# Optimization experiments

Measured on AMD Instinct MI355X. Metric: run time of the kernel, lower is better.

Reference implementation:

```python
import jax, jax.numpy as jnp
import numpy as np

H = 16          # num_attention_heads
HD = 64         # hidden_size_per_attention_head
EPS = 1e-12

def _layernorm(x, w, b):
    u = x.mean(-1, keepdims=True)
    s = ((x - u) ** 2).mean(-1, keepdims=True)
    return w * (x - u) / jnp.sqrt(s + EPS) + b

def _split_heads(x):
    b, s, d = x.shape
    return x.reshape(b, s, H, d // H).transpose(0, 2, 1, 3)  # [b,h,s,hd]

def _merge_heads(x):
    b, h, s, hd = x.shape
    return x.transpose(0, 2, 1, 3).reshape(b, s, h * hd)


def setup_inputs() -> dict:
    key = jax.random.key(0)
    ks = jax.random.split(key, 20)
    B, S, T, D, F = 4, 1024, 1024, 1024, 4096
    w = lambda k, shp: (jax.random.normal(k, shp, jnp.float32) * 0.02)
    return {
        "hidden_states": jax.random.normal(ks[0], (B, S, D), jnp.float32),
        "enc_hidden_states": jax.random.normal(ks[1], (B, T, D), jnp.float32),
        "enc_attn_mask": jnp.zeros((B, 1, 1, T), jnp.float32),
        "dec_attn_mask": jnp.tril(jnp.ones((S, S), jnp.float32)).reshape(1, 1, S, S),
        "ln1_w": jnp.ones((D,), jnp.float32), "ln1_b": jnp.zeros((D,), jnp.float32),
        "qkv_w": w(ks[2], (D, 3 * D)), "qkv_b": jnp.zeros((3 * D,), jnp.float32),
        "attn_o_w": w(ks[3], (D, D)), "attn_o_b": jnp.zeros((D,), jnp.float32),
        "ln2_w": jnp.ones((D,), jnp.float32), "ln2_b": jnp.zeros((D,), jnp.float32),
        "q_w": w(ks[4], (D, D)), "q_b": jnp.zeros((D,), jnp.float32),
        "kv_w": w(ks[5], (D, 2 * D)), "kv_b": jnp.zeros((2 * D,), jnp.float32),
        "ca_o_w": w(ks[6], (D, D)), "ca_o_b": jnp.zeros((D,), jnp.float32),
        "ln3_w": jnp.ones((D,), jnp.float32), "ln3_b": jnp.zeros((D,), jnp.float32),
        "ffn_in_w": w(ks[7], (D, F)), "ffn_in_b": jnp.zeros((F,), jnp.float32),
        "ffn_out_w": w(ks[8], (F, D)), "ffn_out_b": jnp.zeros((D,), jnp.float32),
    }


def reference(hidden_states, enc_hidden_states, enc_attn_mask, dec_attn_mask,
              ln1_w, ln1_b, qkv_w, qkv_b, attn_o_w, attn_o_b,
              ln2_w, ln2_b, q_w, q_b, kv_w, kv_b, ca_o_w, ca_o_b,
              ln3_w, ln3_b, ffn_in_w, ffn_in_b, ffn_out_w, ffn_out_b):
    scale = 1.0 / jnp.sqrt(jnp.float32(HD))
    # dropout layers are identity (eval mode)

    # ---- self-attention (ltor multiplicative mask formula) ----
    residual = hidden_states
    x = _layernorm(hidden_states, ln1_w, ln1_b)
    qkv = x @ qkv_w + qkv_b
    q, k, v = jnp.split(qkv, 3, axis=-1)
    q, k, v = _split_heads(q), _split_heads(k), _split_heads(v)
    scores = jnp.einsum('bhsd,bhtd->bhst', q, k) * scale
    scores = scores * dec_attn_mask - 10000.0 * (1.0 - dec_attn_mask)
    probs = jax.nn.softmax(scores, axis=-1)
    ctx = _merge_heads(jnp.einsum('bhst,bhtd->bhsd', probs, v))
    hidden_states = residual + (ctx @ attn_o_w + attn_o_b)

    # ---- cross-attention (additive enc mask) ----
    residual = hidden_states
    x = _layernorm(hidden_states, ln2_w, ln2_b)
    q = _split_heads(x @ q_w + q_b)
    kv = enc_hidden_states @ kv_w + kv_b
    k, v = jnp.split(kv, 2, axis=-1)
    k, v = _split_heads(k), _split_heads(v)
    scores = jnp.einsum('bhsd,bhtd->bhst', q, k) * scale + enc_attn_mask
    probs = jax.nn.softmax(scores, axis=-1)
    ctx = _merge_heads(jnp.einsum('bhst,bhtd->bhsd', probs, v))
    hidden_states = residual + (ctx @ ca_o_w + ca_o_b)

    # ---- FFN ----
    residual = hidden_states
    x = _layernorm(hidden_states, ln3_w, ln3_b)
    x = jax.nn.gelu(x @ ffn_in_w + ffn_in_b, approximate=False)
    x = x @ ffn_out_w + ffn_out_b
    return residual + x
```

## Files before the change

kernel.cpp:

```cpp
#include <hip/hip_runtime.h>
#include <cstdint>
#include <cstddef>

typedef unsigned short u16;
typedef __bf16 bf16x8 __attribute__((ext_vector_type(8)));
typedef float f32x4 __attribute__((ext_vector_type(4)));

__device__ __forceinline__ u16 f2bf(float f) {
  unsigned u = __float_as_uint(f);
  u += 0x7fffu + ((u >> 16) & 1u);
  return (u16)(u >> 16);
}

__device__ __forceinline__ float block_sum(float v, float* sbuf, int tid) {
#pragma unroll
  for (int off = 1; off < 64; off <<= 1) v += __shfl_xor(v, off, 64);
  if ((tid & 63) == 0) sbuf[tid >> 6] = v;
  __syncthreads();
  v = sbuf[0] + sbuf[1] + sbuf[2] + sbuf[3];
  __syncthreads();
  return v;
}

__device__ __forceinline__ void gld16(const void* g, void* l) {
  __builtin_amdgcn_global_load_lds((const __attribute__((address_space(1))) void*)g,
                                   (__attribute__((address_space(3))) void*)l,
                                   16, 0, 0);
}

__device__ __forceinline__ void swz(int& bx, int& by) {
  const int gx = gridDim.x, gy = gridDim.y;
  const int id = blockIdx.y * gx + blockIdx.x;
  const int xcd = id & 7, slot = id >> 3;
  bx = xcd * (gx >> 3) + slot / gy;
  by = slot % gy;
}


#define GEMM_SETUP(Kdim)                                                         \
  const int lane = tid & 63, wave = tid >> 6;                                    \
  const int l15 = lane & 15, g = (lane >> 4) & 3;                                \
  const int wm = (wave >> 1) * 64, wn = (wave & 1) * 64;                         \
  const int c0 = tid, c1 = tid + 256;                                            \
  const int ar0 = c0 >> 2, ak0 = (c0 & 3) * 8;                                   \
  const int ar1 = c1 >> 2, ak1 = (c1 & 3) * 8;                                   \
  const size_t aoff0 = (size_t)(m0 + ar0) * Kdim + ak0;                          \
  const size_t aoff1 = (size_t)(m0 + ar1) * Kdim + ak1;                          \
  const size_t boff0 = (size_t)(n0 + ar0) * Kdim + ak0;                          \
  const size_t boff1 = (size_t)(n0 + ar1) * Kdim + ak1;

#define GEMM_STAGE(Aptr, Bptr, kk, buf)                                          \
    gld16(Aptr + aoff0 + (kk), As + (buf) * 4096 + (size_t)c0 * 8);              \
    gld16(Aptr + aoff1 + (kk), As + (buf) * 4096 + (size_t)c1 * 8);              \
    gld16(Bptr + boff0 + (kk), Bs + (buf) * 4096 + (size_t)c0 * 8);              \
    gld16(Bptr + boff1 + (kk), Bs + (buf) * 4096 + (size_t)c1 * 8);

#define GEMM_COMPUTE(buf)                                                        \
    { bf16x8 af[4], bg[4];                                                       \
      _Pragma("unroll")                                                          \
      for (int i = 0; i < 4; i++) {                                              \
        af[i] = *(const bf16x8*)(As + (buf) * 4096 + (wm + i * 16 + l15) * 32 + g * 8); \
        bg[i] = *(const bf16x8*)(Bs + (buf) * 4096 + (wn + i * 16 + l15) * 32 + g * 8); \
      }                                                                          \
      _Pragma("unroll")                                                          \
      for (int i = 0; i < 4; i++)                                                \
        _Pragma("unroll")                                                        \
        for (int j = 0; j < 4; j++)                                              \
          acc[i][j] = __builtin_amdgcn_mfma_f32_16x16x32_bf16(af[i], bg[j], acc[i][j], 0, 0, 0); }

#define GEMM_BODY_DB(Aptr, Bptr, Kdim)                                           \
  GEMM_SETUP(Kdim)                                                               \
  f32x4 acc[4][4] = {};                                                          \
  GEMM_STAGE(Aptr, Bptr, kstart, 0)                                              \
  int cur = 0;                                                                   \
  for (int k0 = kstart; k0 + 32 < kend; k0 += 32) {                              \
    GEMM_STAGE(Aptr, Bptr, k0 + 32, cur ^ 1)                                     \
    asm volatile("s_waitcnt vmcnt(4)\ns_barrier" ::: "memory");                  \
    GEMM_COMPUTE(cur)                                                            \
    asm volatile("s_waitcnt lgkmcnt(0)\ns_barrier" ::: "memory");                \
    cur ^= 1;                                                                    \
  }                                                                              \
  asm volatile("s_waitcnt vmcnt(0)\ns_barrier" ::: "memory");                    \
  GEMM_COMPUTE(cur)

template<int BM, int MODE>
__global__ __launch_bounds__(512, 2) void gemm_big(
    const u16* __restrict__ A, const u16* __restrict__ B,
    const float* __restrict__ bias,
    u16* __restrict__ out0, u16* __restrict__ out1, u16* __restrict__ out2,
    int N, int K)
{
  constexpr int NQA = BM / 64;
  constexpr int IF  = BM / 32;
  __shared__ __align__(16) u16 As[2 * BM * 64];
  __shared__ __align__(16) u16 Bs[2 * 256 * 64];

  const int tid = threadIdx.x;
  const int lane = tid & 63, wave = tid >> 6;
  const int l15 = lane & 15, g = (lane >> 4) & 3;
  const int wr = (wave >> 2) * (BM / 2), wc = (wave & 3) * 64;

  const int gx = gridDim.x;
  const int nwg = gx * gridDim.y;
  const int id = blockIdx.y * gx + blockIdx.x;
  const int qq = nwg >> 3, rr = nwg & 7;
  const int xcd = id & 7, slot = id >> 3;
  const int sid = (xcd < rr ? xcd * (qq + 1) : rr * (qq + 1) + (xcd - rr) * qq) + slot;
  const int bx = sid % gx, by = sid / gx;
  const int m0 = by * BM, n0 = bx * 256;

  size_t aoff[NQA]; int adst[NQA];
  size_t boff[4];   int bdst[4];
#pragma unroll
  for (int q = 0; q < NQA; ++q) {
    const int c = tid + q * 512, row = c >> 3, ch = (c & 7) ^ (row & 7);
    aoff[q] = (size_t)(m0 + row) * K + ch * 8;
    adst[q] = c * 8;
  }
#pragma unroll
  for (int q = 0; q < 4; ++q) {
    const int c = tid + q * 512, row = c >> 3, ch = (c & 7) ^ (row & 7);
    boff[q] = (size_t)(n0 + row) * K + ch * 8;
    bdst[q] = c * 8;
  }

#define G2_STAGE(kk, buf)                                                        \
  {                                                                              \
    _Pragma("unroll")                                                            \
    for (int q = 0; q < NQA; ++q) gld16(A + aoff[q] + (kk), As + (buf) * (BM * 64) + adst[q]); \
    _Pragma("unroll")                                                            \
    for (int q = 0; q < 4; ++q)  gld16(B + boff[q] + (kk), Bs + (buf) * 16384 + bdst[q]); \
  }

#define G2_COMPUTE(buf)                                                          \
  {                                                                              \
    _Pragma("unroll")                                                            \
    for (int ks = 0; ks < 2; ++ks) {                                             \
      const int chR = (((ks * 4 + g) ^ (l15 & 7)) * 8);                          \
      bf16x8 af[IF], bg[4];                                                      \
      _Pragma("unroll")                                                          \
      for (int i = 0; i < IF; ++i)                                               \
        af[i] = *(const bf16x8*)(As + (buf) * (BM * 64) + (wr + i * 16 + l15) * 64 + chR); \
      _Pragma("unroll")                                                          \
      for (int j = 0; j < 4; ++j)                                                \
        bg[j] = *(const bf16x8*)(Bs + (buf) * 16384 + (wc + j * 16 + l15) * 64 + chR); \
      _Pragma("unroll")                                                          \
      for (int i = 0; i < IF; ++i)                                               \
        _Pragma("unroll")                                                        \
        for (int j = 0; j < 4; ++j)                                              \
          acc[i][j] = __builtin_amdgcn_mfma_f32_16x16x32_bf16(af[i], bg[j], acc[i][j], 0, 0, 0); \
    }                                                                            \
  }

  f32x4 acc[IF][4] = {};
  const int NT = K >> 6;
  G2_STAGE(0, 0)
  int cur = 0;
  for (int t = 0; t < NT - 1; ++t) {
    G2_STAGE((t + 1) * 64, cur ^ 1)
    if constexpr (BM == 256) asm volatile("s_waitcnt vmcnt(8)\ns_barrier" ::: "memory");
    else                     asm volatile("s_waitcnt vmcnt(6)\ns_barrier" ::: "memory");
    G2_COMPUTE(cur)
    asm volatile("s_waitcnt lgkmcnt(0)\ns_barrier" ::: "memory");
    cur ^= 1;
  }
  asm volatile("s_waitcnt vmcnt(0)\ns_barrier" ::: "memory");
  G2_COMPUTE(cur)

#undef G2_STAGE
#undef G2_COMPUTE

  if constexpr (MODE == 0) {
#pragma unroll
    for (int i = 0; i < IF; ++i) {
#pragma unroll
      for (int j = 0; j < 4; ++j) {
        const int col = n0 + wc + j * 16 + l15;
        const float bs = bias[col];
#pragma unroll
        for (int r = 0; r < 4; ++r) {
          const int gm = m0 + wr + i * 16 + g * 4 + r;
          float v = acc[i][j][r] + bs;
          v = 0.5f * v * (1.0f + erff(v * 0.70710678118654752f));
          out0[(size_t)gm * N + col] = f2bf(v);
        }
      }
    }
  } else {
#pragma unroll
    for (int i = 0; i < IF; ++i) {
#pragma unroll
      for (int j = 0; j < 4; ++j) {
        const int col = n0 + wc + j * 16 + l15;
        const int sec = (n0 + wc + j * 16) >> 10;
        const int tgt = (MODE == 1) ? sec : sec + 1;
        const float bs = bias[col];
#pragma unroll
        for (int r = 0; r < 4; ++r) {
          const int gm = m0 + wr + i * 16 + g * 4 + r;
          const float v = acc[i][j][r] + bs;
          const int cl = col & 1023, h = cl >> 6, d = cl & 63;
          const int z = (gm >> 10) * 16 + h, s = gm & 1023;
          if (tgt == 0)
            out0[((size_t)z * 1024 + s) * 64 + d] = f2bf(v * 0.125f);
          else if (tgt == 1)
            out1[((((size_t)z * 8 + (s >> 7)) * 8 + (d >> 3)) * 128 + (s & 127)) * 8 + (d & 7)] = f2bf(v);
          else
            out2[((size_t)z * 8 + (s >> 7)) * 8192 + (((s >> 3) & 15) * 64 + d) * 8 + (s & 7)] = f2bf(v);
        }
      }
    }
  }
}

__global__ __launch_bounds__(256) void gemm_splitk(
    const u16* __restrict__ A, const u16* __restrict__ B,
    float* __restrict__ part, int K, int Klen)
{
  __shared__ __align__(16) u16 As[2 * 128 * 32];
  __shared__ __align__(16) u16 Bs[2 * 128 * 32];
  const int tid = threadIdx.x;
  int bx, by; swz(bx, by);
  const int m0 = by * 128, n0 = bx * 128;
  const int kstart = blockIdx.z * Klen, kend = kstart + Klen;
  float* outP = part + (size_t)blockIdx.z * (4096ULL * 1024);
  GEMM_BODY_DB(A, B, K)

#pragma unroll
  for (int i = 0; i < 4; i++)
#pragma unroll
    for (int j = 0; j < 4; j++) {
      const int col = n0 + wn + j * 16 + l15;
#pragma unroll
      for (int r = 0; r < 4; r++) {
        const int gm = m0 + wm + i * 16 + g * 4 + r;
        outP[(size_t)gm * 1024 + col] = acc[i][j][r];
      }
    }
}

__global__ __launch_bounds__(256, 2) void flash_attn(
    const u16* __restrict__ qh, const u16* __restrict__ kt, const u16* __restrict__ vt,
    const float* __restrict__ emask, u16* __restrict__ ctx, int causal)
{
  __shared__ __align__(16) u16 sK[8192];
  __shared__ __align__(16) u16 sV[8192];
  __shared__ __align__(16) u16 sP[128 * 72];

  const int tid = threadIdx.x, lane = tid & 63, wave = tid >> 6;
  const int l15 = lane & 15, g = (lane >> 4) & 3;
  const int id = blockIdx.y * 8 + blockIdx.x;
  const int xcd = id & 7, slot = id >> 3;
  const int z = xcd * 8 + (slot >> 3), b = z >> 4, h = z & 15;
  const int m0 = (slot & 7) * 128;
  const int r0 = wave * 32;

  bf16x8 qf[2][2];
  {
    const u16* qz = qh + ((size_t)z * 1024 + m0 + r0 + l15) * 64 + g * 8;
#pragma unroll
    for (int i2 = 0; i2 < 2; ++i2)
#pragma unroll
      for (int kc = 0; kc < 2; ++kc)
        qf[i2][kc] = *(const bf16x8*)(qz + (size_t)i2 * 16 * 64 + kc * 32);
  }

  float m_i[2][4], l_i[2][4];
#pragma unroll
  for (int i2 = 0; i2 < 2; ++i2)
#pragma unroll
    for (int r = 0; r < 4; ++r) { m_i[i2][r] = -1.0e30f; l_i[i2][r] = 0.0f; }

  f32x4 o[2][4] = {};
  const int tmax = causal ? m0 : 896;

  for (int t0 = 0; t0 <= tmax; t0 += 128) {
    const u16* ktile = kt + ((size_t)z * 8 + (t0 >> 7)) * 8192;
    const u16* vtile = vt + ((size_t)z * 8 + (t0 >> 7)) * 8192;
    __syncthreads();
#pragma unroll
    for (int i = 0; i < 4; ++i) {
      const int off = (wave * 4 + i) * 512 + lane * 8;
      gld16(ktile + off, sK + off);
      gld16(vtile + off, sV + off);
    }
    __syncthreads();

#pragma unroll
    for (int ci = 0; ci < 2; ++ci) {
      if (causal && t0 == m0 && ci * 64 > r0 + 31) continue;

      f32x4 sa[2][4] = {};
#pragma unroll
      for (int kc = 0; kc < 2; ++kc) {
        bf16x8 bg[4];
#pragma unroll
        for (int jn = 0; jn < 4; ++jn)
          bg[jn] = *(const bf16x8*)(sK + ((kc * 4 + g) * 128 + ci * 64 + jn * 16 + l15) * 8);
#pragma unroll
        for (int i2 = 0; i2 < 2; ++i2)
#pragma unroll
          for (int jn = 0; jn < 4; ++jn)
            sa[i2][jn] = __builtin_amdgcn_mfma_f32_16x16x32_bf16(qf[i2][kc], bg[jn], sa[i2][jn], 0, 0, 0);
      }

      if (causal) {
        if (t0 == m0 && ci * 64 + 63 > r0) {
#pragma unroll
          for (int i2 = 0; i2 < 2; ++i2)
#pragma unroll
            for (int jn = 0; jn < 4; ++jn) {
              const int col = ci * 64 + jn * 16 + l15;
#pragma unroll
              for (int r = 0; r < 4; ++r) {
                const int row = r0 + i2 * 16 + g * 4 + r;
                if (col > row) sa[i2][jn][r] = -3.0e38f;
              }
            }
        }
      } else {
#pragma unroll
        for (int jn = 0; jn < 4; ++jn) {
          const float mv = emask[(size_t)b * 1024 + t0 + ci * 64 + jn * 16 + l15];
#pragma unroll
          for (int i2 = 0; i2 < 2; ++i2)
#pragma unroll
            for (int r = 0; r < 4; ++r) sa[i2][jn][r] += mv;
        }
      }

      float alpha[2][4];
#pragma unroll
      for (int i2 = 0; i2 < 2; ++i2)
#pragma unroll
        for (int r = 0; r < 4; ++r) {
          const int rowl = r0 + i2 * 16 + g * 4 + r;
          float v = fmaxf(fmaxf(sa[i2][0][r], sa[i2][1][r]), fmaxf(sa[i2][2][r], sa[i2][3][r]));
          v = fmaxf(v, __shfl_xor(v, 1, 64));
          v = fmaxf(v, __shfl_xor(v, 2, 64));
          v = fmaxf(v, __shfl_xor(v, 4, 64));
          v = fmaxf(v, __shfl_xor(v, 8, 64));
          const float mo = m_i[i2][r];
          const float mn = fmaxf(mo, v);
          m_i[i2][r] = mn;
          alpha[i2][r] = __expf(mo - mn);
          float s = 0.0f;
#pragma unroll
          for (int jn = 0; jn < 4; ++jn) {
            const float p = __expf(sa[i2][jn][r] - mn);
            s += p;
            sP[rowl * 72 + jn * 16 + l15] = f2bf(p);
          }
          s += __shfl_xor(s, 1, 64);
          s += __shfl_xor(s, 2, 64);
          s += __shfl_xor(s, 4, 64);
          s += __shfl_xor(s, 8, 64);
          l_i[i2][r] = alpha[i2][r] * l_i[i2][r] + s;
        }

#pragma unroll
      for (int i2 = 0; i2 < 2; ++i2)
#pragma unroll
        for (int jn = 0; jn < 4; ++jn)
#pragma unroll
          for (int r = 0; r < 4; ++r)
            o[i2][jn][r] *= alpha[i2][r];

      asm volatile("s_waitcnt lgkmcnt(0)" ::: "memory");
#pragma unroll
      for (int kc2 = 0; kc2 < 2; ++kc2) {
        bf16x8 pa[2], vb[4];
#pragma unroll
        for (int i2 = 0; i2 < 2; ++i2)
          pa[i2] = *(const bf16x8*)(sP + (r0 + i2 * 16 + l15) * 72 + kc2 * 32 + g * 8);
#pragma unroll
        for (int jn = 0; jn < 4; ++jn)
          vb[jn] = *(const bf16x8*)(sV + ((ci * 8 + kc2 * 4 + g) * 64 + jn * 16 + l15) * 8);
#pragma unroll
        for (int i2 = 0; i2 < 2; ++i2)
#pragma unroll
          for (int jn = 0; jn < 4; ++jn)
            o[i2][jn] = __builtin_amdgcn_mfma_f32_16x16x32_bf16(pa[i2], vb[jn], o[i2][jn], 0, 0, 0);
      }
    }
  }

#pragma unroll
  for (int i2 = 0; i2 < 2; ++i2)
#pragma unroll
    for (int r = 0; r < 4; ++r) {
      const float inv = 1.0f / l_i[i2][r];
      const size_t base = ((size_t)(b * 1024 + m0 + r0 + i2 * 16 + g * 4 + r)) * 1024 + h * 64;
#pragma unroll
      for (int jn = 0; jn < 4; ++jn)
        ctx[base + jn * 16 + l15] = f2bf(o[i2][jn][r] * inv);
    }
}

struct PrepArgs {
  const float* w[7]; u16* wt[7]; int K[7]; int N[7]; int cum[7];
  const float* enc; u16* enc_bf;
  const float* hid; const float* ln1w; const float* ln1b; u16* xln;
};
__global__ __launch_bounds__(256) void prep_kernel(PrepArgs a) {
  __shared__ float t[32][33];
  __shared__ float sbuf[4];
  const int bb = blockIdx.x, tid = threadIdx.x;
  if (bb < 16384) {
    int wi = 0;
#pragma unroll
    for (int i = 0; i < 7; ++i) if (bb >= a.cum[i]) wi = i + 1; else break;
    const int base = wi ? a.cum[wi - 1] : 0;
    const int tileIdx = bb - base;
    const int Kd = a.K[wi], Nd = a.N[wi], nx = Nd >> 5;
    const int n0 = (tileIdx % nx) * 32, k0 = (tileIdx / nx) * 32;
    const float* w = a.w[wi]; u16* wt = a.wt[wi];
    const int tx = tid & 31, ty = tid >> 5;
#pragma unroll
    for (int r = ty; r < 32; r += 8) t[r][tx] = w[(size_t)(k0 + r) * Nd + n0 + tx];
    __syncthreads();
#pragma unroll
    for (int r = ty; r < 32; r += 8) wt[(size_t)(n0 + r) * Kd + k0 + tx] = f2bf(t[tx][r]);
  } else if (bb < 20480) {
    const size_t i = ((size_t)(bb - 16384) * 256 + tid) * 4;
    const float4 v = *(const float4*)(a.enc + i);
    ushort4 o; o.x = f2bf(v.x); o.y = f2bf(v.y); o.z = f2bf(v.z); o.w = f2bf(v.w);
    *(ushort4*)(a.enc_bf + i) = o;
  } else {
    const int row = bb - 20480;
    const float4 v = *(const float4*)(a.hid + (size_t)row * 1024 + tid * 4);
    float s = block_sum(v.x + v.y + v.z + v.w, sbuf, tid);
    const float u = s * (1.0f / 1024.0f);
    const float d0 = v.x - u, d1 = v.y - u, d2 = v.z - u, d3 = v.w - u;
    float sq = block_sum(d0 * d0 + d1 * d1 + d2 * d2 + d3 * d3, sbuf, tid);
    const float rstd = rsqrtf(sq * (1.0f / 1024.0f) + 1e-12f);
    const int c = tid * 4;
    ushort4 o;
    o.x = f2bf(a.ln1w[c + 0] * d0 * rstd + a.ln1b[c + 0]);
    o.y = f2bf(a.ln1w[c + 1] * d1 * rstd + a.ln1b[c + 1]);
    o.z = f2bf(a.ln1w[c + 2] * d2 * rstd + a.ln1b[c + 2]);
    o.w = f2bf(a.ln1w[c + 3] * d3 * rstd + a.ln1b[c + 3]);
    *(ushort4*)(a.xln + (size_t)row * 1024 + c) = o;
  }
}

__global__ __launch_bounds__(256) void ln_red_kernel(
    const float* __restrict__ p0, const float* __restrict__ p1,
    const float* __restrict__ bias, const float* __restrict__ res,
    const float* __restrict__ w, const float* __restrict__ b,
    float* __restrict__ hOut, u16* __restrict__ xln)
{
  __shared__ float sbuf[4];
  const int row = blockIdx.x, tid = threadIdx.x;
  const size_t off = (size_t)row * 1024 + tid * 4;
  const int c = tid * 4;
  const float4 a0 = *(const float4*)(p0 + off);
  const float4 a1 = *(const float4*)(p1 + off);
  const float4 bs = *(const float4*)(bias + c);
  const float4 rs = *(const float4*)(res + off);
  float4 v;
  v.x = a0.x + a1.x + bs.x + rs.x;
  v.y = a0.y + a1.y + bs.y + rs.y;
  v.z = a0.z + a1.z + bs.z + rs.z;
  v.w = a0.w + a1.w + bs.w + rs.w;
  *(float4*)(hOut + off) = v;
  float s = block_sum(v.x + v.y + v.z + v.w, sbuf, tid);
  const float u = s * (1.0f / 1024.0f);
  const float d0 = v.x - u, d1 = v.y - u, d2 = v.z - u, d3 = v.w - u;
  float sq = block_sum(d0 * d0 + d1 * d1 + d2 * d2 + d3 * d3, sbuf, tid);
  const float rstd = rsqrtf(sq * (1.0f / 1024.0f) + 1e-12f);
  ushort4 o;
  o.x = f2bf(w[c + 0] * d0 * rstd + b[c + 0]);
  o.y = f2bf(w[c + 1] * d1 * rstd + b[c + 1]);
  o.z = f2bf(w[c + 2] * d2 * rstd + b[c + 2]);
  o.w = f2bf(w[c + 3] * d3 * rstd + b[c + 3]);
  *(ushort4*)(xln + off) = o;
}

__global__ __launch_bounds__(256) void reduce_q_kernel(
    const float* __restrict__ p0, const float* __restrict__ p1,
    const float* __restrict__ bias, u16* __restrict__ qh)
{
  const int m = blockIdx.x, tid = threadIdx.x;
  const size_t off = (size_t)m * 1024 + tid * 4;
  const int n = tid * 4, h = n >> 6, d = n & 63;
  const int b = m >> 10, s = m & 1023;
  const float4 a0 = *(const float4*)(p0 + off);
  const float4 a1 = *(const float4*)(p1 + off);
  const float4 bs = *(const float4*)(bias + n);
  ushort4 o;
  o.x = f2bf((a0.x + a1.x + bs.x) * 0.125f);
  o.y = f2bf((a0.y + a1.y + bs.y) * 0.125f);
  o.z = f2bf((a0.z + a1.z + bs.z) * 0.125f);
  o.w = f2bf((a0.w + a1.w + bs.w) * 0.125f);
  *(ushort4*)(qh + ((size_t)((b * 16 + h) * 1024 + s)) * 64 + d) = o;
}

__global__ __launch_bounds__(256) void reduce_out_kernel(
    const float* __restrict__ p0, const float* __restrict__ p1,
    const float* __restrict__ bias, const float* __restrict__ res,
    float* __restrict__ out)
{
  const int m = blockIdx.x, tid = threadIdx.x;
  const size_t off = (size_t)m * 1024 + tid * 4;
  const int c = tid * 4;
  const float4 a0 = *(const float4*)(p0 + off);
  const float4 a1 = *(const float4*)(p1 + off);
  const float4 bs = *(const float4*)(bias + c);
  const float4 rs = *(const float4*)(res + off);
  float4 v;
  v.x = a0.x + a1.x + bs.x + rs.x;
  v.y = a0.y + a1.y + bs.y + rs.y;
  v.z = a0.z + a1.z + bs.z + rs.z;
  v.w = a0.w + a1.w + bs.w + rs.w;
  *(float4*)(out + off) = v;
}

constexpr size_t MB = 1024ULL * 1024;
constexpr size_t WT_QKV    = 0;
constexpr size_t WT_ATTN_O = 6 * MB;
constexpr size_t WT_Q      = 8 * MB;
constexpr size_t WT_KV     = 10 * MB;
constexpr size_t WT_CA_O   = 14 * MB;
constexpr size_t WT_FFN_IN = 16 * MB;
constexpr size_t WT_FFN_OUT= 24 * MB;
constexpr size_t ENC_BF    = 32 * MB;
constexpr size_t XLN       = 40 * MB;
constexpr size_t QH        = 48 * MB;
constexpr size_t KT        = 56 * MB;
constexpr size_t VT        = 64 * MB;
constexpr size_t CTX       = 72 * MB;
constexpr size_t HBUF      = 80 * MB;
constexpr size_t SP0       = 96 * MB;
constexpr size_t SP1       = 112 * MB;
constexpr size_t FFN_MID   = 128 * MB;

extern "C" void kernel_launch(void* const* d_in, const int* in_sizes, int n_in,
                              void* d_out, int out_size, void* d_ws, size_t ws_size,
                              hipStream_t stream) {
  const float* hidden   = (const float*)d_in[0];
  const float* enc      = (const float*)d_in[1];
  const float* encm     = (const float*)d_in[2];
  const float* ln1w = (const float*)d_in[4],  *ln1b = (const float*)d_in[5];
  const float* qkv_w = (const float*)d_in[6], *qkv_b = (const float*)d_in[7];
  const float* attn_o_w = (const float*)d_in[8], *attn_o_b = (const float*)d_in[9];
  const float* ln2w = (const float*)d_in[10], *ln2b = (const float*)d_in[11];
  const float* q_w = (const float*)d_in[12],  *q_b = (const float*)d_in[13];
  const float* kv_w = (const float*)d_in[14], *kv_b = (const float*)d_in[15];
  const float* ca_o_w = (const float*)d_in[16], *ca_o_b = (const float*)d_in[17];
  const float* ln3w = (const float*)d_in[18], *ln3b = (const float*)d_in[19];
  const float* ffn_in_w = (const float*)d_in[20], *ffn_in_b = (const float*)d_in[21];
  const float* ffn_out_w = (const float*)d_in[22], *ffn_out_b = (const float*)d_in[23];

  char* ws = (char*)d_ws;
  u16* wt_qkv    = (u16*)(ws + WT_QKV);
  u16* wt_attn_o = (u16*)(ws + WT_ATTN_O);
  u16* wt_q      = (u16*)(ws + WT_Q);
  u16* wt_kv     = (u16*)(ws + WT_KV);
  u16* wt_ca_o   = (u16*)(ws + WT_CA_O);
  u16* wt_ffn_in = (u16*)(ws + WT_FFN_IN);
  u16* wt_ffn_out= (u16*)(ws + WT_FFN_OUT);
  u16* enc_bf = (u16*)(ws + ENC_BF);
  u16* xln    = (u16*)(ws + XLN);
  u16* qh     = (u16*)(ws + QH);
  u16* kt     = (u16*)(ws + KT);
  u16* vt     = (u16*)(ws + VT);
  u16* ctx    = (u16*)(ws + CTX);
  float* hF   = (float*)(ws + HBUF);
  float* sp0  = (float*)(ws + SP0);
  float* sp1  = (float*)(ws + SP1);
  u16* ffn_mid = (u16*)(ws + FFN_MID);

  PrepArgs pa;
  pa.w[0] = qkv_w;    pa.wt[0] = wt_qkv;     pa.K[0] = 1024; pa.N[0] = 3072; pa.cum[0] = 3072;
  pa.w[1] = attn_o_w; pa.wt[1] = wt_attn_o;  pa.K[1] = 1024; pa.N[1] = 1024; pa.cum[1] = 4096;
  pa.w[2] = q_w;      pa.wt[2] = wt_q;       pa.K[2] = 1024; pa.N[2] = 1024; pa.cum[2] = 5120;
  pa.w[3] = kv_w;     pa.wt[3] = wt_kv;      pa.K[3] = 1024; pa.N[3] = 2048; pa.cum[3] = 7168;
  pa.w[4] = ca_o_w;   pa.wt[4] = wt_ca_o;    pa.K[4] = 1024; pa.N[4] = 1024; pa.cum[4] = 8192;
  pa.w[5] = ffn_in_w; pa.wt[5] = wt_ffn_in;  pa.K[5] = 1024; pa.N[5] = 4096; pa.cum[5] = 12288;
  pa.w[6] = ffn_out_w;pa.wt[6] = wt_ffn_out; pa.K[6] = 4096; pa.N[6] = 1024; pa.cum[6] = 16384;
  pa.enc = enc; pa.enc_bf = enc_bf;
  pa.hid = hidden; pa.ln1w = ln1w; pa.ln1b = ln1b; pa.xln = xln;
  prep_kernel<<<24576, 256, 0, stream>>>(pa);

  gemm_big<256, 1><<<dim3(12, 16), 512, 0, stream>>>(xln, wt_qkv, qkv_b, qh, kt, vt, 3072, 1024);
  flash_attn<<<dim3(8, 64), 256, 0, stream>>>(qh, kt, vt, nullptr, ctx, 1);
  gemm_splitk<<<dim3(8, 32, 2), 256, 0, stream>>>(ctx, wt_attn_o, sp0, 1024, 512);
  ln_red_kernel<<<4096, 256, 0, stream>>>(sp0, sp1, attn_o_b, hidden, ln2w, ln2b, hF, xln);

  gemm_splitk<<<dim3(8, 32, 2), 256, 0, stream>>>(xln, wt_q, sp0, 1024, 512);
  reduce_q_kernel<<<4096, 256, 0, stream>>>(sp0, sp1, q_b, qh);
  gemm_big<128, 3><<<dim3(8, 32), 512, 0, stream>>>(enc_bf, wt_kv, kv_b, nullptr, kt, vt, 2048, 1024);
  flash_attn<<<dim3(8, 64), 256, 0, stream>>>(qh, kt, vt, encm, ctx, 0);
  gemm_splitk<<<dim3(8, 32, 2), 256, 0, stream>>>(ctx, wt_ca_o, sp0, 1024, 512);
  ln_red_kernel<<<4096, 256, 0, stream>>>(sp0, sp1, ca_o_b, hF, ln3w, ln3b, hF, xln);

  gemm_big<256, 0><<<dim3(16, 16), 512, 0, stream>>>(xln, wt_ffn_in, ffn_in_b, ffn_mid, nullptr, nullptr, 4096, 1024);
  gemm_splitk<<<dim3(8, 32, 2), 256, 0, stream>>>(ffn_mid, wt_ffn_out, sp0, 4096, 2048);
  reduce_out_kernel<<<4096, 256, 0, stream>>>(sp0, sp1, ffn_out_b, hF, (float*)d_out);
}
```

Baseline: 581.0 us.

## Replace 128x128 split-K GEMMs with big-tile swizzled GEMM, drop split-K for D×D

The old 128x128, K=32 split-K kernel is replaced by a templated gemm_part that reuses the big-GEMM machinery: 512 threads, a 256-column tile, K=64 steps with XOR-swizzled LDS and XCD-aware block remapping. The three D×D projections now run without split-K (BM=64, 256 blocks), so the reduction kernels read a single partial buffer instead of summing two. The FFN-out GEMM keeps a 2-way split with BM=128. Fewer blocks and no split for the small GEMMs lower parallelism, traded against less partial-buffer traffic and better reuse per tile.

```diff
diff --git a/kernel.cpp b/kernel.cpp
--- a/kernel.cpp
+++ b/kernel.cpp
@@ -28,111 +28,47 @@
                                    16, 0, 0);
 }
 
-__device__ __forceinline__ void swz(int& bx, int& by) {
-  const int gx = gridDim.x, gy = gridDim.y;
-  const int id = blockIdx.y * gx + blockIdx.x;
-  const int xcd = id & 7, slot = id >> 3;
-  bx = xcd * (gx >> 3) + slot / gy;
-  by = slot % gy;
-}
-
-
-#define GEMM_SETUP(Kdim)                                                         \
+
+
+#define BIG_PREAMBLE(BM, Kdim, KB)                                               \
+  constexpr int NQA = (BM) / 64;                                                 \
+  constexpr int IF  = (BM) / 32;                                                 \
+  const int tid = threadIdx.x;                                                   \
   const int lane = tid & 63, wave = tid >> 6;                                    \
   const int l15 = lane & 15, g = (lane >> 4) & 3;                                \
-  const int wm = (wave >> 1) * 64, wn = (wave & 1) * 64;                         \
-  const int c0 = tid, c1 = tid + 256;                                            \
-  const int ar0 = c0 >> 2, ak0 = (c0 & 3) * 8;                                   \
-  const int ar1 = c1 >> 2, ak1 = (c1 & 3) * 8;                                   \
-  const size_t aoff0 = (size_t)(m0 + ar0) * Kdim + ak0;                          \
-  const size_t aoff1 = (size_t)(m0 + ar1) * Kdim + ak1;                          \
-  const size_t boff0 = (size_t)(n0 + ar0) * Kdim + ak0;                          \
-  const size_t boff1 = (size_t)(n0 + ar1) * Kdim + ak1;
-
-#define GEMM_STAGE(Aptr, Bptr, kk, buf)                                          \
-    gld16(Aptr + aoff0 + (kk), As + (buf) * 4096 + (size_t)c0 * 8);              \
-    gld16(Aptr + aoff1 + (kk), As + (buf) * 4096 + (size_t)c1 * 8);              \
-    gld16(Bptr + boff0 + (kk), Bs + (buf) * 4096 + (size_t)c0 * 8);              \
-    gld16(Bptr + boff1 + (kk), Bs + (buf) * 4096 + (size_t)c1 * 8);
-
-#define GEMM_COMPUTE(buf)                                                        \
-    { bf16x8 af[4], bg[4];                                                       \
-      _Pragma("unroll")                                                          \
-      for (int i = 0; i < 4; i++) {                                              \
-        af[i] = *(const bf16x8*)(As + (buf) * 4096 + (wm + i * 16 + l15) * 32 + g * 8); \
-        bg[i] = *(const bf16x8*)(Bs + (buf) * 4096 + (wn + i * 16 + l15) * 32 + g * 8); \
-      }                                                                          \
-      _Pragma("unroll")                                                          \
-      for (int i = 0; i < 4; i++)                                                \
-        _Pragma("unroll")                                                        \
-        for (int j = 0; j < 4; j++)                                              \
-          acc[i][j] = __builtin_amdgcn_mfma_f32_16x16x32_bf16(af[i], bg[j], acc[i][j], 0, 0, 0); }
-
-#define GEMM_BODY_DB(Aptr, Bptr, Kdim)                                           \
-  GEMM_SETUP(Kdim)                                                               \
-  f32x4 acc[4][4] = {};                                                          \
-  GEMM_STAGE(Aptr, Bptr, kstart, 0)                                              \
-  int cur = 0;                                                                   \
-  for (int k0 = kstart; k0 + 32 < kend; k0 += 32) {                              \
-    GEMM_STAGE(Aptr, Bptr, k0 + 32, cur ^ 1)                                     \
-    asm volatile("s_waitcnt vmcnt(4)\ns_barrier" ::: "memory");                  \
-    GEMM_COMPUTE(cur)                                                            \
-    asm volatile("s_waitcnt lgkmcnt(0)\ns_barrier" ::: "memory");                \
-    cur ^= 1;                                                                    \
+  const int wr = (wave >> 2) * ((BM) / 2), wc = (wave & 3) * 64;                 \
+  const int gx = gridDim.x;                                                      \
+  const int nwg = gx * gridDim.y;                                                \
+  const int id = blockIdx.y * gx + blockIdx.x;                                   \
+  const int qq = nwg >> 3, rr = nwg & 7;                                         \
+  const int xcd = id & 7, slot = id >> 3;                                        \
+  const int sid = (xcd < rr ? xcd * (qq + 1) : rr * (qq + 1) + (xcd - rr) * qq) + slot; \
+  const int bx = sid % gx, by = sid / gx;                                        \
+  const int m0 = by * (BM), n0 = bx * 256;                                       \
+  size_t aoff[NQA]; int adst[NQA];                                               \
+  size_t boff[4];   int bdst[4];                                                 \
+  _Pragma("unroll")                                                              \
+  for (int q = 0; q < NQA; ++q) {                                                \
+    const int c = tid + q * 512, row = c >> 3, ch = (c & 7) ^ (row & 7);         \
+    aoff[q] = (size_t)(m0 + row) * (Kdim) + ch * 8 + (KB);                       \
+    adst[q] = c * 8;                                                             \
   }                                                                              \
-  asm volatile("s_waitcnt vmcnt(0)\ns_barrier" ::: "memory");                    \
-  GEMM_COMPUTE(cur)
-
-template<int BM, int MODE>
-__global__ __launch_bounds__(512, 2) void gemm_big(
-    const u16* __restrict__ A, const u16* __restrict__ B,
-    const float* __restrict__ bias,
-    u16* __restrict__ out0, u16* __restrict__ out1, u16* __restrict__ out2,
-    int N, int K)
-{
-  constexpr int NQA = BM / 64;
-  constexpr int IF  = BM / 32;
-  __shared__ __align__(16) u16 As[2 * BM * 64];
-  __shared__ __align__(16) u16 Bs[2 * 256 * 64];
-
-  const int tid = threadIdx.x;
-  const int lane = tid & 63, wave = tid >> 6;
-  const int l15 = lane & 15, g = (lane >> 4) & 3;
-  const int wr = (wave >> 2) * (BM / 2), wc = (wave & 3) * 64;
-
-  const int gx = gridDim.x;
-  const int nwg = gx * gridDim.y;
-  const int id = blockIdx.y * gx + blockIdx.x;
-  const int qq = nwg >> 3, rr = nwg & 7;
-  const int xcd = id & 7, slot = id >> 3;
-  const int sid = (xcd < rr ? xcd * (qq + 1) : rr * (qq + 1) + (xcd - rr) * qq) + slot;
-  const int bx = sid % gx, by = sid / gx;
-  const int m0 = by * BM, n0 = bx * 256;
-
-  size_t aoff[NQA]; int adst[NQA];
-  size_t boff[4];   int bdst[4];
-#pragma unroll
-  for (int q = 0; q < NQA; ++q) {
-    const int c = tid + q * 512, row = c >> 3, ch = (c & 7) ^ (row & 7);
-    aoff[q] = (size_t)(m0 + row) * K + ch * 8;
-    adst[q] = c * 8;
-  }
-#pragma unroll
-  for (int q = 0; q < 4; ++q) {
-    const int c = tid + q * 512, row = c >> 3, ch = (c & 7) ^ (row & 7);
-    boff[q] = (size_t)(n0 + row) * K + ch * 8;
-    bdst[q] = c * 8;
-  }
-
-#define G2_STAGE(kk, buf)                                                        \
+  _Pragma("unroll")                                                              \
+  for (int q = 0; q < 4; ++q) {                                                  \
+    const int c = tid + q * 512, row = c >> 3, ch = (c & 7) ^ (row & 7);         \
+    boff[q] = (size_t)(n0 + row) * (Kdim) + ch * 8 + (KB);                       \
+    bdst[q] = c * 8;                                                             \
+  }
+
+#define BIG_STAGE(BM, kk, buf)                                                   \
   {                                                                              \
     _Pragma("unroll")                                                            \
-    for (int q = 0; q < NQA; ++q) gld16(A + aoff[q] + (kk), As + (buf) * (BM * 64) + adst[q]); \
+    for (int q = 0; q < NQA; ++q) gld16(A + aoff[q] + (kk), As + (buf) * ((BM) * 64) + adst[q]); \
     _Pragma("unroll")                                                            \
     for (int q = 0; q < 4; ++q)  gld16(B + boff[q] + (kk), Bs + (buf) * 16384 + bdst[q]); \
   }
 
-#define G2_COMPUTE(buf)                                                          \
+#define BIG_COMPUTE(BM, buf)                                                     \
   {                                                                              \
     _Pragma("unroll")                                                            \
     for (int ks = 0; ks < 2; ++ks) {                                             \
@@ -140,7 +76,7 @@
       bf16x8 af[IF], bg[4];                                                      \
       _Pragma("unroll")                                                          \
       for (int i = 0; i < IF; ++i)                                               \
-        af[i] = *(const bf16x8*)(As + (buf) * (BM * 64) + (wr + i * 16 + l15) * 64 + chR); \
+        af[i] = *(const bf16x8*)(As + (buf) * ((BM) * 64) + (wr + i * 16 + l15) * 64 + chR); \
       _Pragma("unroll")                                                          \
       for (int j = 0; j < 4; ++j)                                                \
         bg[j] = *(const bf16x8*)(Bs + (buf) * 16384 + (wc + j * 16 + l15) * 64 + chR); \
@@ -152,23 +88,37 @@
     }                                                                            \
   }
 
-  f32x4 acc[IF][4] = {};
+#define BIG_WAIT_PREV(BM)                                                        \
+  if constexpr ((BM) == 256)      asm volatile("s_waitcnt vmcnt(8)\ns_barrier" ::: "memory"); \
+  else if constexpr ((BM) == 128) asm volatile("s_waitcnt vmcnt(6)\ns_barrier" ::: "memory"); \
+  else                            asm volatile("s_waitcnt vmcnt(5)\ns_barrier" ::: "memory");
+
+#define BIG_KLOOP(BM, NT)                                                        \
+  f32x4 acc[IF][4] = {};                                                         \
+  BIG_STAGE(BM, 0, 0)                                                            \
+  int cur = 0;                                                                   \
+  for (int t = 0; t < (NT) - 1; ++t) {                                           \
+    BIG_STAGE(BM, (t + 1) * 64, cur ^ 1)                                         \
+    BIG_WAIT_PREV(BM)                                                            \
+    BIG_COMPUTE(BM, cur)                                                         \
+    asm volatile("s_waitcnt lgkmcnt(0)\ns_barrier" ::: "memory");                \
+    cur ^= 1;                                                                    \
+  }                                                                              \
+  asm volatile("s_waitcnt vmcnt(0)\ns_barrier" ::: "memory");                    \
+  BIG_COMPUTE(BM, cur)
+
+template<int BM, int MODE>
+__global__ __launch_bounds__(512, 2) void gemm_big(
+    const u16* __restrict__ A, const u16* __restrict__ B,
+    const float* __restrict__ bias,
+    u16* __restrict__ out0, u16* __restrict__ out1, u16* __restrict__ out2,
+    int N, int K)
+{
+  __shared__ __align__(16) u16 As[2 * BM * 64];
+  __shared__ __align__(16) u16 Bs[2 * 256 * 64];
+  BIG_PREAMBLE(BM, K, 0)
   const int NT = K >> 6;
-  G2_STAGE(0, 0)
-  int cur = 0;
-  for (int t = 0; t < NT - 1; ++t) {
-    G2_STAGE((t + 1) * 64, cur ^ 1)
-    if constexpr (BM == 256) asm volatile("s_waitcnt vmcnt(8)\ns_barrier" ::: "memory");
-    else                     asm volatile("s_waitcnt vmcnt(6)\ns_barrier" ::: "memory");
-    G2_COMPUTE(cur)
-    asm volatile("s_waitcnt lgkmcnt(0)\ns_barrier" ::: "memory");
-    cur ^= 1;
-  }
-  asm volatile("s_waitcnt vmcnt(0)\ns_barrier" ::: "memory");
-  G2_COMPUTE(cur)
-
-#undef G2_STAGE
-#undef G2_COMPUTE
+  BIG_KLOOP(BM, NT)
 
   if constexpr (MODE == 0) {
 #pragma unroll
@@ -213,27 +163,27 @@
   }
 }
 
-__global__ __launch_bounds__(256) void gemm_splitk(
+template<int BM>
+__global__ __launch_bounds__(512, 2) void gemm_part(
     const u16* __restrict__ A, const u16* __restrict__ B,
     float* __restrict__ part, int K, int Klen)
 {
-  __shared__ __align__(16) u16 As[2 * 128 * 32];
-  __shared__ __align__(16) u16 Bs[2 * 128 * 32];
-  const int tid = threadIdx.x;
-  int bx, by; swz(bx, by);
-  const int m0 = by * 128, n0 = bx * 128;
-  const int kstart = blockIdx.z * Klen, kend = kstart + Klen;
+  __shared__ __align__(16) u16 As[2 * BM * 64];
+  __shared__ __align__(16) u16 Bs[2 * 256 * 64];
+  const int kb = blockIdx.z * Klen;
   float* outP = part + (size_t)blockIdx.z * (4096ULL * 1024);
-  GEMM_BODY_DB(A, B, K)
-
-#pragma unroll
-  for (int i = 0; i < 4; i++)
-#pragma unroll
-    for (int j = 0; j < 4; j++) {
-      const int col = n0 + wn + j * 16 + l15;
-#pragma unroll
-      for (int r = 0; r < 4; r++) {
-        const int gm = m0 + wm + i * 16 + g * 4 + r;
+  BIG_PREAMBLE(BM, K, kb)
+  const int NT = Klen >> 6;
+  BIG_KLOOP(BM, NT)
+
+#pragma unroll
+  for (int i = 0; i < IF; ++i)
+#pragma unroll
+    for (int j = 0; j < 4; ++j) {
+      const int col = n0 + wc + j * 16 + l15;
+#pragma unroll
+      for (int r = 0; r < 4; ++r) {
+        const int gm = m0 + wr + i * 16 + g * 4 + r;
         outP[(size_t)gm * 1024 + col] = acc[i][j][r];
       }
     }
@@ -444,8 +394,8 @@
   }
 }
 
-__global__ __launch_bounds__(256) void ln_red_kernel(
-    const float* __restrict__ p0, const float* __restrict__ p1,
+__global__ __launch_bounds__(256) void ln_red1_kernel(
+    const float* __restrict__ p0,
     const float* __restrict__ bias, const float* __restrict__ res,
     const float* __restrict__ w, const float* __restrict__ b,
     float* __restrict__ hOut, u16* __restrict__ xln)
@@ -455,14 +405,13 @@
   const size_t off = (size_t)row * 1024 + tid * 4;
   const int c = tid * 4;
   const float4 a0 = *(const float4*)(p0 + off);
-  const float4 a1 = *(const float4*)(p1 + off);
   const float4 bs = *(const float4*)(bias + c);
   const float4 rs = *(const float4*)(res + off);
   float4 v;
-  v.x = a0.x + a1.x + bs.x + rs.x;
-  v.y = a0.y + a1.y + bs.y + rs.y;
-  v.z = a0.z + a1.z + bs.z + rs.z;
-  v.w = a0.w + a1.w + bs.w + rs.w;
+  v.x = a0.x + bs.x + rs.x;
+  v.y = a0.y + bs.y + rs.y;
+  v.z = a0.z + bs.z + rs.z;
+  v.w = a0.w + bs.w + rs.w;
   *(float4*)(hOut + off) = v;
   float s = block_sum(v.x + v.y + v.z + v.w, sbuf, tid);
   const float u = s * (1.0f / 1024.0f);
@@ -477,8 +426,8 @@
   *(ushort4*)(xln + off) = o;
 }
 
-__global__ __launch_bounds__(256) void reduce_q_kernel(
-    const float* __restrict__ p0, const float* __restrict__ p1,
+__global__ __launch_bounds__(256) void reduce_q1_kernel(
+    const float* __restrict__ p0,
     const float* __restrict__ bias, u16* __restrict__ qh)
 {
   const int m = blockIdx.x, tid = threadIdx.x;
@@ -486,13 +435,12 @@
   const int n = tid * 4, h = n >> 6, d = n & 63;
   const int b = m >> 10, s = m & 1023;
   const float4 a0 = *(const float4*)(p0 + off);
-  const float4 a1 = *(const float4*)(p1 + off);
   const float4 bs = *(const float4*)(bias + n);
   ushort4 o;
-  o.x = f2bf((a0.x + a1.x + bs.x) * 0.125f);
-  o.y = f2bf((a0.y + a1.y + bs.y) * 0.125f);
-  o.z = f2bf((a0.z + a1.z + bs.z) * 0.125f);
-  o.w = f2bf((a0.w + a1.w + bs.w) * 0.125f);
+  o.x = f2bf((a0.x + bs.x) * 0.125f);
+  o.y = f2bf((a0.y + bs.y) * 0.125f);
+  o.z = f2bf((a0.z + bs.z) * 0.125f);
+  o.w = f2bf((a0.w + bs.w) * 0.125f);
   *(ushort4*)(qh + ((size_t)((b * 16 + h) * 1024 + s)) * 64 + d) = o;
 }
 
@@ -585,17 +533,17 @@
 
   gemm_big<256, 1><<<dim3(12, 16), 512, 0, stream>>>(xln, wt_qkv, qkv_b, qh, kt, vt, 3072, 1024);
   flash_attn<<<dim3(8, 64), 256, 0, stream>>>(qh, kt, vt, nullptr, ctx, 1);
-  gemm_splitk<<<dim3(8, 32, 2), 256, 0, stream>>>(ctx, wt_attn_o, sp0, 1024, 512);
-  ln_red_kernel<<<4096, 256, 0, stream>>>(sp0, sp1, attn_o_b, hidden, ln2w, ln2b, hF, xln);
-
-  gemm_splitk<<<dim3(8, 32, 2), 256, 0, stream>>>(xln, wt_q, sp0, 1024, 512);
-  reduce_q_kernel<<<4096, 256, 0, stream>>>(sp0, sp1, q_b, qh);
+  gemm_part<64><<<dim3(4, 64, 1), 512, 0, stream>>>(ctx, wt_attn_o, sp0, 1024, 1024);
+  ln_red1_kernel<<<4096, 256, 0, stream>>>(sp0, attn_o_b, hidden, ln2w, ln2b, hF, xln);
+
+  gemm_part<64><<<dim3(4, 64, 1), 512, 0, stream>>>(xln, wt_q, sp0, 1024, 1024);
+  reduce_q1_kernel<<<4096, 256, 0, stream>>>(sp0, q_b, qh);
   gemm_big<128, 3><<<dim3(8, 32), 512, 0, stream>>>(enc_bf, wt_kv, kv_b, nullptr, kt, vt, 2048, 1024);
   flash_attn<<<dim3(8, 64), 256, 0, stream>>>(qh, kt, vt, encm, ctx, 0);
-  gemm_splitk<<<dim3(8, 32, 2), 256, 0, stream>>>(ctx, wt_ca_o, sp0, 1024, 512);
-  ln_red_kernel<<<4096, 256, 0, stream>>>(sp0, sp1, ca_o_b, hF, ln3w, ln3b, hF, xln);
+  gemm_part<64><<<dim3(4, 64, 1), 512, 0, stream>>>(ctx, wt_ca_o, sp0, 1024, 1024);
+  ln_red1_kernel<<<4096, 256, 0, stream>>>(sp0, ca_o_b, hF, ln3w, ln3b, hF, xln);
 
   gemm_big<256, 0><<<dim3(16, 16), 512, 0, stream>>>(xln, wt_ffn_in, ffn_in_b, ffn_mid, nullptr, nullptr, 4096, 1024);
-  gemm_splitk<<<dim3(8, 32, 2), 256, 0, stream>>>(ffn_mid, wt_ffn_out, sp0, 4096, 2048);
+  gemm_part<128><<<dim3(4, 32, 2), 512, 0, stream>>>(ffn_mid, wt_ffn_out, sp0, 4096, 2048);
   reduce_out_kernel<<<4096, 256, 0, stream>>>(sp0, sp1, ffn_out_b, hF, (float*)d_out);
 }
```

Result: faster. 555.4 us (-4.4%).
